# Optimization experiments

Measured on AMD Instinct MI355X. Metric: run time of the kernel, lower is better.

The kernel has to match this reference:

```python
import jax, jax.numpy as jnp
import numpy as np

SIM_THRESHOLD = 0.7  # suppression threshold on cosine similarity


def setup_inputs() -> dict:
    key = jax.random.key(0)
    k1, k2 = jax.random.split(key)
    tokens = jax.random.normal(k1, (4, 4096, 256), dtype=jnp.float32)
    scores = jax.random.uniform(k2, (4, 4096), dtype=jnp.float32)
    return {"tokens": tokens, "scores": scores}


def _nms_keep_sorted(sim_sorted):
    """Greedy NMS over tokens already sorted by descending score.

    sim_sorted: [N, N] pairwise cosine similarity in sorted order.
    Returns keep mask [N] (bool) in sorted order.
    """
    N = sim_sorted.shape[0]
    idx = jnp.arange(N)

    def step(suppressed, i):
        keep_i = jnp.logical_not(suppressed[i])
        row = sim_sorted[i]  # similarity of token i to all tokens
        # a kept token suppresses all later (lower-score) similar tokens
        suppressed = suppressed | (keep_i & (row > SIM_THRESHOLD) & (idx > i))
        return suppressed, keep_i

    _, keeps = jax.lax.scan(step, jnp.zeros(N, dtype=bool), idx)
    return keeps


def reference(tokens, scores):
    # tokens: [B, N, D], scores: [B, N]
    t = tokens / (jnp.linalg.norm(tokens, axis=-1, keepdims=True) + 1e-6)
    sim = jnp.einsum('bnd,bmd->bnm', t, t)  # [B, N, N] cosine similarity
    order = jnp.argsort(-scores, axis=-1)   # descending score order

    def per_batch(sim_b, order_b):
        sim_sorted = sim_b[order_b][:, order_b]          # reorder rows+cols
        keeps_sorted = _nms_keep_sorted(sim_sorted)      # [N] bool, sorted order
        keep = jnp.zeros_like(keeps_sorted).at[order_b].set(keeps_sorted)
        return keep

    keep = jax.vmap(per_batch)(sim, order)               # [B, N] bool
    masked_tokens = tokens * keep[..., None].astype(tokens.dtype)
    return masked_tokens, keep
```

## Files before the change

kernel.cpp:

```cpp
#include <hip/hip_runtime.h>

#define BATCH 4
#define N 4096
#define D 256
#define THR 0.7f
#define CAP 4096

typedef __attribute__((ext_vector_type(8))) short bf16x8;
typedef __attribute__((ext_vector_type(4))) float f32x4;

__device__ __forceinline__ unsigned short f2bf(float f) {
    unsigned int u = __float_as_uint(f);
    unsigned int r = (u + 0x7FFFu + ((u >> 16) & 1u)) >> 16;
    return (unsigned short)r;
}

__device__ __forceinline__ unsigned int fflip(float f) {
    unsigned int u = __float_as_uint(f);
    return (u & 0x80000000u) ? ~u : (u | 0x80000000u);
}

__device__ __forceinline__ void gl_lds16(const unsigned short* g, unsigned short* l) {
    __builtin_amdgcn_global_load_lds(
        (const __attribute__((address_space(1))) unsigned int*)g,
        (__attribute__((address_space(3))) unsigned int*)l, 16, 0, 0);
}

__global__ __launch_bounds__(256) void norm_kernel(const float* __restrict__ tokens,
                                                   unsigned short* __restrict__ ts,
                                                   int* __restrict__ cnt) {
    if (blockIdx.x == 0 && threadIdx.x < BATCH) cnt[threadIdx.x] = 0;
    int gw = (int)((blockIdx.x * 256 + threadIdx.x) >> 6);
    int lane = threadIdx.x & 63;
    const float4* p = (const float4*)(tokens + (size_t)gw * D);
    float4 v = p[lane];
    float ss = v.x * v.x + v.y * v.y + v.z * v.z + v.w * v.w;
#pragma unroll
    for (int off = 32; off > 0; off >>= 1) ss += __shfl_xor(ss, off);
    float inv = 1.0f / (sqrtf(ss) + 1e-6f);
    ushort4 pk;
    pk.x = f2bf(v.x * inv);
    pk.y = f2bf(v.y * inv);
    pk.z = f2bf(v.z * inv);
    pk.w = f2bf(v.w * inv);
    *((ushort4*)(ts + (size_t)gw * D + lane * 4)) = pk;
}

__global__ __launch_bounds__(256, 3) void sim_kernel(const unsigned short* __restrict__ ts,
                                                     const float* __restrict__ scores,
                                                     unsigned long long* __restrict__ edges,
                                                     int* __restrict__ cnt) {
    __shared__ unsigned short smem[16384];
    int b = blockIdx.y;
    int ti = blockIdx.x >> 5;
    int tj = blockIdx.x & 31;
    if (tj < ti) return;

    int t = threadIdx.x;
    int w = t >> 6;
    int L = t & 63;
    const unsigned short* base = ts + (size_t)b * N * D;

    int r = L >> 3, c = L & 7;
    const unsigned short* pa = base + (size_t)(ti * 128 + w * 8 + r) * D + (c ^ r) * 8;
    const unsigned short* pb = base + (size_t)(tj * 128 + w * 8 + r) * D + (c ^ r) * 8;
    unsigned short* la = smem + w * 512;
    unsigned short* lb = smem + 8192 + w * 512;

    int wr = w >> 1, wc = w & 1;
    int m = L & 15, q = L >> 4;
    int slot0 = ((q ^ (m & 7))) * 8;
    int a_base = (wr * 64 + m) * 64;
    int b_base = 8192 + (wc * 64 + m) * 64;

    f32x4 acc[4][4] = {};

    for (int s = 0; s < 4; ++s) {
#pragma unroll
        for (int i = 0; i < 4; ++i) {
            gl_lds16(pa + i * 32 * D, la + i * 2048);
            gl_lds16(pb + i * 32 * D, lb + i * 2048);
        }
        pa += 64; pb += 64;
        __syncthreads();
#pragma unroll
        for (int sub = 0; sub < 2; ++sub) {
            int slot = slot0 ^ (sub * 32);
            bf16x8 af[4], bf[4];
#pragma unroll
            for (int f = 0; f < 4; ++f) {
                af[f] = *(const bf16x8*)(smem + a_base + f * 1024 + slot);
                bf[f] = *(const bf16x8*)(smem + b_base + f * 1024 + slot);
            }
#pragma unroll
            for (int fa = 0; fa < 4; ++fa)
#pragma unroll
                for (int fb = 0; fb < 4; ++fb)
                    acc[fa][fb] = __builtin_amdgcn_mfma_f32_16x16x32_bf16(
                        af[fa], bf[fb], acc[fa][fb], 0, 0, 0);
        }
        __syncthreads();
    }

    int rbase = q * 4;
#pragma unroll
    for (int fa = 0; fa < 4; ++fa) {
#pragma unroll
        for (int fb = 0; fb < 4; ++fb) {
#pragma unroll
            for (int rr = 0; rr < 4; ++rr) {
                int ig = ti * 128 + wr * 64 + fa * 16 + rbase + rr;
                int jg = tj * 128 + wc * 64 + fb * 16 + m;
                if (jg > ig && acc[fa][fb][rr] > THR) {
                    float si = scores[b * N + ig];
                    float sj = scores[b * N + jg];
                    int src, dst;
                    float ssrc;
                    if (si >= sj) { src = ig; dst = jg; ssrc = si; }
                    else          { src = jg; dst = ig; ssrc = sj; }
                    int pos = atomicAdd(&cnt[b], 1);
                    if (pos < CAP) {
                        unsigned long long kk =
                            ((unsigned long long)fflip(ssrc) << 24) |
                            ((unsigned long long)(unsigned int)(4095 - src) << 12) |
                            (unsigned long long)(unsigned int)dst;
                        edges[b * CAP + pos] = kk;
                    }
                }
            }
        }
    }
}

__global__ __launch_bounds__(256) void nms_kernel(const unsigned long long* __restrict__ edges,
                                                  const int* __restrict__ cnt,
                                                  float* __restrict__ keep_out) {
    int b = blockIdx.x;
    __shared__ unsigned long long e[CAP];
    __shared__ unsigned int sup[N / 32];
    int n = cnt[b];
    if (n > CAP) n = CAP;
    for (int i = threadIdx.x; i < N / 32; i += 256) sup[i] = 0u;
    if (n > 0) {
        for (int i = threadIdx.x; i < CAP; i += 256)
            e[i] = (i < n) ? edges[b * CAP + i] : 0ull;
        __syncthreads();
        for (int k = 2; k <= CAP; k <<= 1) {
            for (int j = k >> 1; j > 0; j >>= 1) {
                for (int i = threadIdx.x; i < CAP; i += 256) {
                    int ixj = i ^ j;
                    if (ixj > i) {
                        unsigned long long a = e[i], cc = e[ixj];
                        bool up = ((i & k) == 0);
                        if (up ? (a < cc) : (a > cc)) { e[i] = cc; e[ixj] = a; }
                    }
                }
                __syncthreads();
            }
        }
        if (threadIdx.x == 0) {
            for (int tt = 0; tt < n; ++tt) {
                unsigned long long u = e[tt];
                int src = 4095 - (int)((u >> 12) & 0xFFFu);
                int dst = (int)(u & 0xFFFu);
                if (!((sup[src >> 5] >> (src & 31)) & 1u))
                    sup[dst >> 5] |= 1u << (dst & 31);
            }
        }
    }
    __syncthreads();
    for (int i = threadIdx.x; i < N; i += 256) {
        bool s = (sup[i >> 5] >> (i & 31)) & 1u;
        keep_out[b * N + i] = s ? 0.0f : 1.0f;
    }
}

__global__ __launch_bounds__(256) void mask_kernel(const float* __restrict__ tokens,
                                                   const float* __restrict__ keep,
                                                   float* __restrict__ out) {
    size_t idx = (size_t)blockIdx.x * 256 + threadIdx.x;
    float4 v = ((const float4*)tokens)[idx];
    float kf = keep[idx >> 6];
    float4 o;
    o.x = v.x * kf; o.y = v.y * kf; o.z = v.z * kf; o.w = v.w * kf;
    ((float4*)out)[idx] = o;
}

extern "C" void kernel_launch(void* const* d_in, const int* in_sizes, int n_in,
                              void* d_out, int out_size, void* d_ws, size_t ws_size,
                              hipStream_t stream) {
    const float* tokens = (const float*)d_in[0];
    const float* scores = (const float*)d_in[1];

    char* ws = (char*)d_ws;
    int* cnt = (int*)ws;
    unsigned long long* edges = (unsigned long long*)(ws + 128);
    unsigned short* ts = (unsigned short*)(ws + 128 + BATCH * CAP * 8);

    float* out = (float*)d_out;
    float* keep_out = out + (size_t)BATCH * N * D;

    norm_kernel<<<(BATCH * N) / 4, 256, 0, stream>>>(tokens, ts, cnt);
    dim3 g(32 * 32, BATCH);
    sim_kernel<<<g, 256, 0, stream>>>(ts, scores, edges, cnt);
    nms_kernel<<<BATCH, 256, 0, stream>>>(edges, cnt, keep_out);
    mask_kernel<<<(BATCH * N * D / 4) / 256, 256, 0, stream>>>(tokens, keep_out, out);
}
```

Before: 106.2 us.

## Use 32x32x16 MFMA and launch only upper-triangular tile blocks

```diff
diff --git a/kernel.cpp b/kernel.cpp
--- a/kernel.cpp
+++ b/kernel.cpp
@@ -7,7 +7,7 @@
 #define CAP 4096
 
 typedef __attribute__((ext_vector_type(8))) short bf16x8;
-typedef __attribute__((ext_vector_type(4))) float f32x4;
+typedef __attribute__((ext_vector_type(16))) float f32x16;
 
 __device__ __forceinline__ unsigned short f2bf(float f) {
     unsigned int u = __float_as_uint(f);
@@ -46,15 +46,17 @@
     *((ushort4*)(ts + (size_t)gw * D + lane * 4)) = pk;
 }
 
-__global__ __launch_bounds__(256, 3) void sim_kernel(const unsigned short* __restrict__ ts,
+__global__ __launch_bounds__(256, 4) void sim_kernel(const unsigned short* __restrict__ ts,
                                                      const float* __restrict__ scores,
                                                      unsigned long long* __restrict__ edges,
                                                      int* __restrict__ cnt) {
     __shared__ unsigned short smem[16384];
+    int p = blockIdx.x;
     int b = blockIdx.y;
-    int ti = blockIdx.x >> 5;
-    int tj = blockIdx.x & 31;
-    if (tj < ti) return;
+    int ti = (int)(32.5f - sqrtf(32.5f * 32.5f - 2.0f * (float)p));
+    while (32 * ti - ti * (ti - 1) / 2 > p) --ti;
+    while (32 * (ti + 1) - (ti + 1) * ti / 2 <= p) ++ti;
+    int tj = ti + (p - (32 * ti - ti * (ti - 1) / 2));
 
     int t = threadIdx.x;
     int w = t >> 6;
@@ -68,12 +70,12 @@
     unsigned short* lb = smem + 8192 + w * 512;
 
     int wr = w >> 1, wc = w & 1;
-    int m = L & 15, q = L >> 4;
-    int slot0 = ((q ^ (m & 7))) * 8;
-    int a_base = (wr * 64 + m) * 64;
-    int b_base = 8192 + (wc * 64 + m) * 64;
-
-    f32x4 acc[4][4] = {};
+    int m = L & 31, h = L >> 5;
+    int arow0 = (wr * 64 + m) * 64;
+    int brow0 = 8192 + (wc * 64 + m) * 64;
+    int swz = m & 7;
+
+    f32x16 acc[2][2] = {};
 
     for (int s = 0; s < 4; ++s) {
 #pragma unroll
@@ -84,34 +86,31 @@
         pa += 64; pb += 64;
         __syncthreads();
 #pragma unroll
-        for (int sub = 0; sub < 2; ++sub) {
-            int slot = slot0 ^ (sub * 32);
-            bf16x8 af[4], bf[4];
-#pragma unroll
-            for (int f = 0; f < 4; ++f) {
-                af[f] = *(const bf16x8*)(smem + a_base + f * 1024 + slot);
-                bf[f] = *(const bf16x8*)(smem + b_base + f * 1024 + slot);
-            }
-#pragma unroll
-            for (int fa = 0; fa < 4; ++fa)
-#pragma unroll
-                for (int fb = 0; fb < 4; ++fb)
-                    acc[fa][fb] = __builtin_amdgcn_mfma_f32_16x16x32_bf16(
-                        af[fa], bf[fb], acc[fa][fb], 0, 0, 0);
+        for (int sub = 0; sub < 4; ++sub) {
+            int slot = (((sub << 1) | h) ^ swz) * 8;
+            bf16x8 a0 = *(const bf16x8*)(smem + arow0 + slot);
+            bf16x8 a1 = *(const bf16x8*)(smem + arow0 + 2048 + slot);
+            bf16x8 b0 = *(const bf16x8*)(smem + brow0 + slot);
+            bf16x8 b1 = *(const bf16x8*)(smem + brow0 + 2048 + slot);
+            acc[0][0] = __builtin_amdgcn_mfma_f32_32x32x16_bf16(a0, b0, acc[0][0], 0, 0, 0);
+            acc[0][1] = __builtin_amdgcn_mfma_f32_32x32x16_bf16(a0, b1, acc[0][1], 0, 0, 0);
+            acc[1][0] = __builtin_amdgcn_mfma_f32_32x32x16_bf16(a1, b0, acc[1][0], 0, 0, 0);
+            acc[1][1] = __builtin_amdgcn_mfma_f32_32x32x16_bf16(a1, b1, acc[1][1], 0, 0, 0);
         }
         __syncthreads();
     }
 
-    int rbase = q * 4;
-#pragma unroll
-    for (int fa = 0; fa < 4; ++fa) {
-#pragma unroll
-        for (int fb = 0; fb < 4; ++fb) {
-#pragma unroll
-            for (int rr = 0; rr < 4; ++rr) {
-                int ig = ti * 128 + wr * 64 + fa * 16 + rbase + rr;
-                int jg = tj * 128 + wc * 64 + fb * 16 + m;
-                if (jg > ig && acc[fa][fb][rr] > THR) {
+#pragma unroll
+    for (int fa = 0; fa < 2; ++fa) {
+#pragma unroll
+        for (int fb = 0; fb < 2; ++fb) {
+#pragma unroll
+            for (int reg = 0; reg < 16; ++reg) {
+                int row = (reg & 3) + 8 * (reg >> 2) + 4 * h;
+                int ig = ti * 128 + wr * 64 + fa * 32 + row;
+                int jg = tj * 128 + wc * 64 + fb * 32 + m;
+                float v = acc[fa][fb][reg];
+                if (jg > ig && v > THR) {
                     float si = scores[b * N + ig];
                     float sj = scores[b * N + jg];
                     int src, dst;
@@ -201,7 +200,7 @@
     float* keep_out = out + (size_t)BATCH * N * D;
 
     norm_kernel<<<(BATCH * N) / 4, 256, 0, stream>>>(tokens, ts, cnt);
-    dim3 g(32 * 32, BATCH);
+    dim3 g(528, BATCH);
     sim_kernel<<<g, 256, 0, stream>>>(ts, scores, edges, cnt);
     nms_kernel<<<BATCH, 256, 0, stream>>>(edges, cnt, keep_out);
     mask_kernel<<<(BATCH * N * D / 4) / 256, 256, 0, stream>>>(tokens, keep_out, out);
```

Measured after the change: 99.92 us. -5.9%, faster.
